# Kernel optimization log

Measured on AMD Instinct MI355X. Metric: run time of the kernel, lower is better.

Reference implementation:

```python
import jax, jax.numpy as jnp
import numpy as np

B, N, DH = 8, 2048, 512
EPS = 1e-5


def _layer_norm(x, g, b):
    m = x.mean(-1, keepdims=True)
    v = ((x - m) ** 2).mean(-1, keepdims=True)
    return (x - m) * jax.lax.rsqrt(v + EPS) * g + b


def setup_inputs() -> dict:
    key = jax.random.key(0)
    ks = jax.random.split(key, 20)
    s = 1.0 / np.sqrt(DH)
    sf = 1.0 / np.sqrt(2 * DH)
    return {
        "H": jax.random.normal(ks[0], (B, N, DH), jnp.float32),
        "adj": jax.random.uniform(ks[1], (B, N, N), jnp.float32),
        "hop_emb": jax.random.normal(ks[2], (N, DH), jnp.float32),
        "Wq": jax.random.normal(ks[3], (DH, DH), jnp.float32) * s,
        "bq": jnp.zeros((DH,), jnp.float32),
        "Wk": jax.random.normal(ks[4], (DH, DH), jnp.float32) * s,
        "bk": jnp.zeros((DH,), jnp.float32),
        "Wv": jax.random.normal(ks[5], (DH, DH), jnp.float32) * s,
        "bv": jnp.zeros((DH,), jnp.float32),
        "W1": jax.random.normal(ks[6], (DH, 2 * DH), jnp.float32) * s,
        "b1": jnp.zeros((2 * DH,), jnp.float32),
        "W2": jax.random.normal(ks[7], (2 * DH, DH), jnp.float32) * sf,
        "b2": jnp.zeros((DH,), jnp.float32),
        "g1": jnp.ones((DH,), jnp.float32),
        "be1": jnp.zeros((DH,), jnp.float32),
        "g2": jnp.ones((DH,), jnp.float32),
        "be2": jnp.zeros((DH,), jnp.float32),
    }


def reference(H, adj, hop_emb, Wq, bq, Wk, bk, Wv, bv, W1, b1, W2, b2, g1, be1, g2, be2):
    Q = H @ Wq + bq                                     # [B,N,DH]
    K = H @ Wk + bk
    V = H @ Wv + bv
    scores = jnp.einsum("bid,bjd->bij", Q, K) / np.sqrt(DH).astype(np.float32)
    # (adj[...,None] * hop_emb).mean(-1) == adj * hop_emb.mean(-1)[j]
    hop_effect = adj * hop_emb.mean(-1)[None, None, :]  # [B,N,N]
    attn = jax.nn.softmax(scores * hop_effect, axis=-1)
    attn_out = jnp.einsum("bij,bjd->bid", attn, V)
    x = _layer_norm(attn_out + H, g1, be1)
    ffn = jax.nn.relu(x @ W1 + b1) @ W2 + b2
    return _layer_norm(ffn + x, g2, be2)
```

## Files before the change

### kernel.cpp

```cpp
#include <hip/hip_runtime.h>

typedef unsigned short u16;
typedef __bf16 bf16x8 __attribute__((ext_vector_type(8)));
typedef float f32x4 __attribute__((ext_vector_type(4)));

#define SEQN 2048
#define DHID 512

static __device__ __forceinline__ float bf2f(u16 u) {
    union { unsigned int i; float f; } c; c.i = ((unsigned int)u) << 16; return c.f;
}
static __device__ __forceinline__ u16 f2bf(float f) {
    union { float f; unsigned int i; } c; c.f = f;
    unsigned int x = c.i;
    return (u16)((x + 0x7fffu + ((x >> 16) & 1u)) >> 16);
}

static __device__ __forceinline__ void gld_lds16(const u16* g, u16* l) {
    __builtin_amdgcn_global_load_lds(
        (__attribute__((address_space(1))) void*)(g),
        (__attribute__((address_space(3))) void*)(l), 16, 0, 0);
}

__global__ __launch_bounds__(256) void cvt_kernel(const float* __restrict__ src,
                                                  u16* __restrict__ dst, int n) {
    int i = (blockIdx.x * 256 + threadIdx.x) * 8;
    if (i >= n) return;
    float4 a = *(const float4*)(src + i);
    float4 b = *(const float4*)(src + i + 4);
    union { uint4 u; u16 s[8]; } o;
    o.s[0] = f2bf(a.x); o.s[1] = f2bf(a.y); o.s[2] = f2bf(a.z); o.s[3] = f2bf(a.w);
    o.s[4] = f2bf(b.x); o.s[5] = f2bf(b.y); o.s[6] = f2bf(b.z); o.s[7] = f2bf(b.w);
    *(uint4*)(dst + i) = o.u;
}

__global__ __launch_bounds__(256) void cvt_t_kernel(const float* __restrict__ src,
                                                    u16* __restrict__ dst, int K, int N) {
    int idx = blockIdx.x * 256 + threadIdx.x;
    if (idx >= K * N) return;
    int n = idx / K, k = idx - n * K;
    dst[idx] = f2bf(src[(size_t)k * N + n]);
}

__global__ void hmean_kernel(const float* __restrict__ hop, float* __restrict__ hm) {
    int j = blockIdx.x, t = threadIdx.x;
    const float* p = hop + (size_t)j * DHID + t * 8;
    float4 a = *(const float4*)p;
    float4 b = *(const float4*)(p + 4);
    float s = a.x + a.y + a.z + a.w + b.x + b.y + b.z + b.w;
#pragma unroll
    for (int m = 1; m < 64; m <<= 1) s += __shfl_xor(s, m);
    if (t == 0) hm[j] = s * (1.0f / (float)DHID);
}

enum { EPI_BIAS = 0, EPI_RELU = 1, EPI_PLAIN = 3, EPI_BIAS_T = 4, EPI_QKV = 5 };

template <int EPI>
__global__ __launch_bounds__(256) void gemm_bt(
    const u16* __restrict__ A, const u16* __restrict__ Bt, u16* __restrict__ C,
    const float* __restrict__ bias,
    int K, int lda, int ldb, int ldc,
    u16* __restrict__ Qo, u16* __restrict__ Ko, u16* __restrict__ Vto,
    const float* __restrict__ bq_, const float* __restrict__ bk_,
    const float* __restrict__ bv_)
{
    __shared__ u16 As[2][128 * 32];
    __shared__ u16 Bs[2][128 * 32];

    const int tid = threadIdx.x;
    const u16* Ab = A;
    const u16* Bb = Bt;

    const int bm0 = blockIdx.y * 128, bn0 = blockIdx.x * 128;
    const int wid = tid >> 6, lane = tid & 63, quad = lane >> 4, l16 = lane & 15;
    const int wm = (wid >> 1) * 64, wn = (wid & 1) * 64;
    const int srow = lane >> 2;
    const int skof = (lane & 3) * 8;

    f32x4 acc[4][4];
#pragma unroll
    for (int i = 0; i < 4; ++i)
#pragma unroll
        for (int j = 0; j < 4; ++j) acc[i][j] = (f32x4){0.f, 0.f, 0.f, 0.f};

#pragma unroll
    for (int it = 0; it < 2; ++it) {
        int c = wid * 2 + it;
        gld_lds16(Ab + (size_t)(bm0 + c * 16 + srow) * lda + skof, &As[0][c * 512]);
    }
#pragma unroll
    for (int it = 0; it < 2; ++it) {
        int c = wid * 2 + it;
        gld_lds16(Bb + (size_t)(bn0 + c * 16 + srow) * ldb + skof, &Bs[0][c * 512]);
    }

    int cur = 0;
    for (int k0 = 0; k0 < K; k0 += 32, cur ^= 1) {
        __syncthreads();

        if (k0 + 32 < K) {
#pragma unroll
            for (int it = 0; it < 2; ++it) {
                int c = wid * 2 + it;
                gld_lds16(Ab + (size_t)(bm0 + c * 16 + srow) * lda + k0 + 32 + skof,
                          &As[cur ^ 1][c * 512]);
            }
#pragma unroll
            for (int it = 0; it < 2; ++it) {
                int c = wid * 2 + it;
                gld_lds16(Bb + (size_t)(bn0 + c * 16 + srow) * ldb + k0 + 32 + skof,
                          &Bs[cur ^ 1][c * 512]);
            }
        }
        __builtin_amdgcn_sched_barrier(0);

        bf16x8 af[4], bfr[4];
#pragma unroll
        for (int i = 0; i < 4; ++i)
            af[i] = *(const bf16x8*)&As[cur][(wm + i * 16 + l16) * 32 + quad * 8];
#pragma unroll
        for (int j = 0; j < 4; ++j)
            bfr[j] = *(const bf16x8*)&Bs[cur][(wn + j * 16 + l16) * 32 + quad * 8];
#pragma unroll
        for (int i = 0; i < 4; ++i)
#pragma unroll
            for (int j = 0; j < 4; ++j)
                acc[i][j] = __builtin_amdgcn_mfma_f32_16x16x32_bf16(af[i], bfr[j], acc[i][j], 0, 0, 0);
    }

#pragma unroll
    for (int i = 0; i < 4; ++i) {
#pragma unroll
        for (int j = 0; j < 4; ++j) {
            const int gn = bn0 + wn + j * 16 + l16;
            const int gm0 = bm0 + wm + i * 16 + quad * 4;
            if constexpr (EPI == EPI_BIAS || EPI == EPI_RELU) {
                const float b = bias[gn];
#pragma unroll
                for (int r = 0; r < 4; ++r) {
                    float v = acc[i][j][r] + b;
                    if constexpr (EPI == EPI_RELU) v = fmaxf(v, 0.f);
                    C[(size_t)(gm0 + r) * ldc + gn] = f2bf(v);
                }
            } else if constexpr (EPI == EPI_BIAS_T) {
                const float b = bias[gn];
                const int bb = gm0 >> 11, n = gm0 & 2047;
                ushort4 o;
                o.x = f2bf(acc[i][j][0] + b);
                o.y = f2bf(acc[i][j][1] + b);
                o.z = f2bf(acc[i][j][2] + b);
                o.w = f2bf(acc[i][j][3] + b);
                *(ushort4*)&C[((size_t)bb * 512 + gn) * 2048 + n] = o;
            } else if constexpr (EPI == EPI_QKV) {
                const int sel = gn >> 9;
                const int n = gn & 511;
                if (sel == 0) {
                    const float b = bq_[n];
#pragma unroll
                    for (int r = 0; r < 4; ++r)
                        Qo[(size_t)(gm0 + r) * DHID + n] = f2bf(acc[i][j][r] + b);
                } else if (sel == 1) {
                    const float b = bk_[n];
#pragma unroll
                    for (int r = 0; r < 4; ++r)
                        Ko[(size_t)(gm0 + r) * DHID + n] = f2bf(acc[i][j][r] + b);
                } else {
                    const float b = bv_[n];
                    const int bb = gm0 >> 11, nn2 = gm0 & 2047;
                    ushort4 o;
                    o.x = f2bf(acc[i][j][0] + b);
                    o.y = f2bf(acc[i][j][1] + b);
                    o.z = f2bf(acc[i][j][2] + b);
                    o.w = f2bf(acc[i][j][3] + b);
                    *(ushort4*)&Vto[((size_t)bb * 512 + n) * 2048 + nn2] = o;
                }
            } else {
#pragma unroll
                for (int r = 0; r < 4; ++r)
                    C[(size_t)(gm0 + r) * ldc + gn] = f2bf(acc[i][j][r]);
            }
        }
    }
}

__global__ __launch_bounds__(256, 2) void attn_kernel(
    const u16* __restrict__ Q, const u16* __restrict__ K, const u16* __restrict__ Vt,
    const float* __restrict__ adj, const float* __restrict__ hm,
    u16* __restrict__ AO)
{
    extern __shared__ u16 lds[];
    u16* Ks = lds;
    u16* Vs = lds + 16384;
    u16* Pb = lds + 32768;

    const int tid = threadIdx.x, wid = tid >> 6, lane = tid & 63;
    const int quad = lane >> 4, l16 = lane & 15;
    const int b = blockIdx.x;
    const int q0 = blockIdx.y * 32 + (wid >> 1) * 16;
    const int ch = wid & 1;
    const int D0 = ch * 256;
    const int srow = lane >> 2, sko = (lane & 3) * 8;

    const u16* Qg = Q + (size_t)b * SEQN * DHID;
    const u16* Kg = K + (size_t)b * SEQN * DHID;
    const u16* Vg = Vt + (size_t)b * DHID * SEQN;
    const float* adjg = adj + (size_t)b * SEQN * SEQN;
    u16* AOg = AO + (size_t)b * SEQN * DHID;
    const float* arow = adjg + (size_t)(q0 + quad * 4) * SEQN;
    u16* Pg = Pb + (wid >> 1) * 640;

    const float scale = 0.044194173824159216f;

    bf16x8 qf[16];
#pragma unroll
    for (int ds = 0; ds < 16; ++ds)
        qf[ds] = *(const bf16x8*)(Qg + (size_t)(q0 + l16) * DHID + ds * 32 + quad * 8);

    f32x4 oacc[16];
#pragma unroll
    for (int dt = 0; dt < 16; ++dt) oacc[dt] = (f32x4){0.f, 0.f, 0.f, 0.f};
    float lsum[4] = {0.f, 0.f, 0.f, 0.f};

#pragma unroll
    for (int i = 0; i < 8; ++i) {
        int id = wid * 8 + i, ds = id >> 1, c = id & 1;
        gld_lds16(Kg + (size_t)(c * 16 + srow) * DHID + ds * 32 + sko,
                  &Ks[ds * 1024 + c * 512]);
    }

    for (int kt = 0; kt < 64; ++kt) {
        const int kv0 = kt * 32;

        __syncthreads();

#pragma unroll
        for (int i = 0; i < 8; ++i) {
            int id = wid * 8 + i;
            gld_lds16(Vg + (size_t)(id * 16 + srow) * SEQN + kv0 + sko,
                      &Vs[id * 512]);
        }

        float hv = hm[kv0 + ch * 16 + l16] * scale;
        float av[4];
#pragma unroll
        for (int r = 0; r < 4; ++r)
            av[r] = arow[(size_t)r * SEQN + kv0 + ch * 16 + l16];

        f32x4 sa = {0.f,0.f,0.f,0.f}, sb = {0.f,0.f,0.f,0.f};
#pragma unroll
        for (int ds = 0; ds < 16; ds += 2) {
            bf16x8 k0 = *(const bf16x8*)&Ks[ds * 1024 + ch * 512 + l16 * 32 + quad * 8];
            sa = __builtin_amdgcn_mfma_f32_16x16x32_bf16(qf[ds], k0, sa, 0, 0, 0);
            bf16x8 k1 = *(const bf16x8*)&Ks[(ds + 1) * 1024 + ch * 512 + l16 * 32 + quad * 8];
            sb = __builtin_amdgcn_mfma_f32_16x16x32_bf16(qf[ds + 1], k1, sb, 0, 0, 0);
        }
        f32x4 s = sa + sb;

        __syncthreads();

        if (kt < 63) {
#pragma unroll
            for (int i = 0; i < 8; ++i) {
                int id = wid * 8 + i, ds = id >> 1, c = id & 1;
                gld_lds16(Kg + (size_t)(kv0 + 32 + c * 16 + srow) * DHID + ds * 32 + sko,
                          &Ks[ds * 1024 + c * 512]);
            }
        }
        __builtin_amdgcn_sched_barrier(0);

#pragma unroll
        for (int r = 0; r < 4; ++r) {
            float p = __expf(s[r] * av[r] * hv);
            lsum[r] += p;
            Pg[(quad * 4 + r) * 40 + ch * 16 + l16] = f2bf(p);
        }

        asm volatile("s_waitcnt lgkmcnt(0)" ::: "memory");
        __builtin_amdgcn_s_barrier();
        __builtin_amdgcn_sched_barrier(0);

        bf16x8 pf = *(const bf16x8*)&Pg[l16 * 40 + quad * 8];

#pragma unroll
        for (int dt = 0; dt < 16; ++dt) {
            bf16x8 vf = *(const bf16x8*)&Vs[(D0 + dt * 16 + l16) * 32 + quad * 8];
            oacc[dt] = __builtin_amdgcn_mfma_f32_16x16x32_bf16(pf, vf, oacc[dt], 0, 0, 0);
        }
    }

#pragma unroll
    for (int r = 0; r < 4; ++r) {
#pragma unroll
        for (int m = 1; m < 16; m <<= 1) lsum[r] += __shfl_xor(lsum[r], m);
    }
    __syncthreads();
    float* SUMS = (float*)Pb;
    if (l16 == 0) {
#pragma unroll
        for (int r = 0; r < 4; ++r) SUMS[wid * 16 + quad * 4 + r] = lsum[r];
    }
    __syncthreads();
#pragma unroll
    for (int r = 0; r < 4; ++r)
        lsum[r] = 1.f / (lsum[r] + SUMS[(wid ^ 1) * 16 + quad * 4 + r]);

#pragma unroll
    for (int dt = 0; dt < 16; ++dt) {
#pragma unroll
        for (int r = 0; r < 4; ++r) {
            AOg[(size_t)(q0 + quad * 4 + r) * DHID + D0 + dt * 16 + l16] =
                f2bf(oacc[dt][r] * lsum[r]);
        }
    }
}

__global__ __launch_bounds__(256) void ln_hf32_kernel(
    const u16* __restrict__ a, const float* __restrict__ Hf,
    const float* __restrict__ g, const float* __restrict__ be,
    u16* __restrict__ out)
{
    size_t row = blockIdx.x;
    int t = threadIdx.x, wid = t >> 6, lane = t & 63;
    unsigned int va = *(const unsigned int*)(a + row * (size_t)DHID + t * 2);
    float2 h = *(const float2*)(Hf + row * (size_t)DHID + t * 2);
    float x0 = bf2f((u16)(va & 0xffff)) + h.x;
    float x1 = bf2f((u16)(va >> 16)) + h.y;
    float s = x0 + x1, sq = x0 * x0 + x1 * x1;
#pragma unroll
    for (int m = 1; m < 64; m <<= 1) { s += __shfl_xor(s, m); sq += __shfl_xor(sq, m); }
    __shared__ float rs[4], rq[4];
    if (lane == 0) { rs[wid] = s; rq[wid] = sq; }
    __syncthreads();
    s = rs[0] + rs[1] + rs[2] + rs[3];
    sq = rq[0] + rq[1] + rq[2] + rq[3];
    float mean = s * (1.f / (float)DHID);
    float var = sq * (1.f / (float)DHID) - mean * mean;
    float rstd = rsqrtf(var + 1e-5f);
    float2 vg = *(const float2*)(g + t * 2);
    float2 vbe = *(const float2*)(be + t * 2);
    float y0 = (x0 - mean) * rstd * vg.x + vbe.x;
    float y1 = (x1 - mean) * rstd * vg.y + vbe.y;
    unsigned int o = (unsigned int)f2bf(y0) | ((unsigned int)f2bf(y1) << 16);
    *(unsigned int*)(out + row * (size_t)DHID + t * 2) = o;
}

__global__ __launch_bounds__(256) void ln_kernel_f32out(
    const u16* __restrict__ a, const u16* __restrict__ bp,
    const float* __restrict__ g, const float* __restrict__ be,
    float* __restrict__ out)
{
    size_t row = blockIdx.x;
    int t = threadIdx.x, wid = t >> 6, lane = t & 63;
    unsigned int va = *(const unsigned int*)(a + row * (size_t)DHID + t * 2);
    unsigned int vb = *(const unsigned int*)(bp + row * (size_t)DHID + t * 2);
    float x0 = bf2f((u16)(va & 0xffff)) + bf2f((u16)(vb & 0xffff));
    float x1 = bf2f((u16)(va >> 16)) + bf2f((u16)(vb >> 16));
    float s = x0 + x1, sq = x0 * x0 + x1 * x1;
#pragma unroll
    for (int m = 1; m < 64; m <<= 1) { s += __shfl_xor(s, m); sq += __shfl_xor(sq, m); }
    __shared__ float rs[4], rq[4];
    if (lane == 0) { rs[wid] = s; rq[wid] = sq; }
    __syncthreads();
    s = rs[0] + rs[1] + rs[2] + rs[3];
    sq = rq[0] + rq[1] + rq[2] + rq[3];
    float mean = s * (1.f / (float)DHID);
    float var = sq * (1.f / (float)DHID) - mean * mean;
    float rstd = rsqrtf(var + 1e-5f);
    float2 vg = *(const float2*)(g + t * 2);
    float2 vbe = *(const float2*)(be + t * 2);
    float y0 = (x0 - mean) * rstd * vg.x + vbe.x;
    float y1 = (x1 - mean) * rstd * vg.y + vbe.y;
    *(float2*)(out + row * (size_t)DHID + t * 2) = make_float2(y0, y1);
}

extern "C" void kernel_launch(void* const* d_in, const int* in_sizes, int n_in,
                              void* d_out, int out_size, void* d_ws, size_t ws_size,
                              hipStream_t stream) {
    const float* H   = (const float*)d_in[0];
    const float* adj = (const float*)d_in[1];
    const float* hop = (const float*)d_in[2];
    const float* Wq  = (const float*)d_in[3];
    const float* bq  = (const float*)d_in[4];
    const float* Wk  = (const float*)d_in[5];
    const float* bk  = (const float*)d_in[6];
    const float* Wv  = (const float*)d_in[7];
    const float* bv  = (const float*)d_in[8];
    const float* W1  = (const float*)d_in[9];
    const float* b1  = (const float*)d_in[10];
    const float* W2  = (const float*)d_in[11];
    const float* b2  = (const float*)d_in[12];
    const float* g1  = (const float*)d_in[13];
    const float* be1 = (const float*)d_in[14];
    const float* g2  = (const float*)d_in[15];
    const float* be2 = (const float*)d_in[16];

    const size_t MiB = 1ull << 20;
    char* w = (char*)d_ws;
    float* hm   = (float*)w;
    u16* Hb    = (u16*)(w + 1 * MiB);
    u16* Wqkvt = (u16*)(w + 17 * MiB);
    u16* W1t   = (u16*)(w + 18 * MiB + 512 * 1024);
    u16* W2t   = (u16*)(w + 19 * MiB + 512 * 1024);
    u16* Q     = (u16*)(w + 21 * MiB);
    u16* Kb    = (u16*)(w + 37 * MiB);
    u16* Vt    = (u16*)(w + 53 * MiB);
    u16* AO    = (u16*)(w + 69 * MiB);
    u16* HID   = (u16*)(w + 85 * MiB);
    u16* X   = Kb;
    u16* F2  = Vt;

    const int BN = 8, N = SEQN, D = DHID;

    cvt_kernel<<<(BN * N * D) / (8 * 256), 256, 0, stream>>>(H, Hb, BN * N * D);
    cvt_t_kernel<<<(D * D + 255) / 256, 256, 0, stream>>>(Wq, Wqkvt, D, D);
    cvt_t_kernel<<<(D * D + 255) / 256, 256, 0, stream>>>(Wk, Wqkvt + D * D, D, D);
    cvt_t_kernel<<<(D * D + 255) / 256, 256, 0, stream>>>(Wv, Wqkvt + 2 * D * D, D, D);
    cvt_t_kernel<<<(D * 2 * D + 255) / 256, 256, 0, stream>>>(W1, W1t, D, 2 * D);
    cvt_t_kernel<<<(2 * D * D + 255) / 256, 256, 0, stream>>>(W2, W2t, 2 * D, D);

    hmean_kernel<<<N, 64, 0, stream>>>(hop, hm);

    gemm_bt<EPI_QKV><<<dim3(12, 128, 1), 256, 0, stream>>>(
        Hb, Wqkvt, nullptr, nullptr, D, D, D, 0, Q, Kb, Vt, bq, bk, bv);

    attn_kernel<<<dim3(8, 64), 256, 68096, stream>>>(Q, Kb, Vt, adj, hm, AO);

    ln_hf32_kernel<<<BN * N, 256, 0, stream>>>(AO, H, g1, be1, X);

    gemm_bt<EPI_RELU><<<dim3(8, 128, 1), 256, 0, stream>>>(
        X, W1t, HID, b1, D, D, D, 2 * D, nullptr, nullptr, nullptr, nullptr, nullptr, nullptr);

    gemm_bt<EPI_BIAS><<<dim3(4, 128, 1), 256, 0, stream>>>(
        HID, W2t, F2, b2, 2 * D, 2 * D, 2 * D, D, nullptr, nullptr, nullptr, nullptr, nullptr, nullptr);

    ln_kernel_f32out<<<BN * N, 256, 0, stream>>>(F2, X, g2, be2, (float*)d_out);
}
```

Baseline: 549.8 us.

## Fuse residual+LayerNorm into attention epilogue and merge prep kernels

```diff
diff --git a/kernel.cpp b/kernel.cpp
--- a/kernel.cpp
+++ b/kernel.cpp
@@ -22,35 +22,49 @@
         (__attribute__((address_space(3))) void*)(l), 16, 0, 0);
 }
 
-__global__ __launch_bounds__(256) void cvt_kernel(const float* __restrict__ src,
-                                                  u16* __restrict__ dst, int n) {
-    int i = (blockIdx.x * 256 + threadIdx.x) * 8;
-    if (i >= n) return;
-    float4 a = *(const float4*)(src + i);
-    float4 b = *(const float4*)(src + i + 4);
-    union { uint4 u; u16 s[8]; } o;
-    o.s[0] = f2bf(a.x); o.s[1] = f2bf(a.y); o.s[2] = f2bf(a.z); o.s[3] = f2bf(a.w);
-    o.s[4] = f2bf(b.x); o.s[5] = f2bf(b.y); o.s[6] = f2bf(b.z); o.s[7] = f2bf(b.w);
-    *(uint4*)(dst + i) = o.u;
-}
-
-__global__ __launch_bounds__(256) void cvt_t_kernel(const float* __restrict__ src,
-                                                    u16* __restrict__ dst, int K, int N) {
-    int idx = blockIdx.x * 256 + threadIdx.x;
-    if (idx >= K * N) return;
-    int n = idx / K, k = idx - n * K;
-    dst[idx] = f2bf(src[(size_t)k * N + n]);
-}
-
-__global__ void hmean_kernel(const float* __restrict__ hop, float* __restrict__ hm) {
-    int j = blockIdx.x, t = threadIdx.x;
-    const float* p = hop + (size_t)j * DHID + t * 8;
-    float4 a = *(const float4*)p;
-    float4 b = *(const float4*)(p + 4);
-    float s = a.x + a.y + a.z + a.w + b.x + b.y + b.z + b.w;
-#pragma unroll
-    for (int m = 1; m < 64; m <<= 1) s += __shfl_xor(s, m);
-    if (t == 0) hm[j] = s * (1.0f / (float)DHID);
+__global__ __launch_bounds__(256) void prep_kernel(
+    const float* __restrict__ H, const float* __restrict__ Wq,
+    const float* __restrict__ Wk, const float* __restrict__ Wv,
+    const float* __restrict__ W1, const float* __restrict__ W2,
+    const float* __restrict__ hop,
+    u16* __restrict__ Hb, u16* __restrict__ Wqkvt,
+    u16* __restrict__ W1t, u16* __restrict__ W2t, float* __restrict__ hm)
+{
+    const int bid = blockIdx.x, tid = threadIdx.x;
+    if (bid < 4096) {
+        int i = (bid * 256 + tid) * 8;
+        float4 a = *(const float4*)(H + i);
+        float4 c = *(const float4*)(H + i + 4);
+        union { uint4 u; u16 s[8]; } o;
+        o.s[0] = f2bf(a.x); o.s[1] = f2bf(a.y); o.s[2] = f2bf(a.z); o.s[3] = f2bf(a.w);
+        o.s[4] = f2bf(c.x); o.s[5] = f2bf(c.y); o.s[6] = f2bf(c.z); o.s[7] = f2bf(c.w);
+        *(uint4*)(Hb + i) = o.u;
+    } else if (bid < 7168) {
+        int idx = (bid - 4096) * 256 + tid;
+        int which = idx >> 18;
+        int rem = idx & 262143;
+        int n = rem >> 9, k = rem & 511;
+        const float* src = (which == 0) ? Wq : ((which == 1) ? Wk : Wv);
+        Wqkvt[idx] = f2bf(src[(size_t)k * 512 + n]);
+    } else if (bid < 9216) {
+        int idx = (bid - 7168) * 256 + tid;
+        int n = idx >> 9, k = idx & 511;
+        W1t[idx] = f2bf(W1[(size_t)k * 1024 + n]);
+    } else if (bid < 11264) {
+        int idx = (bid - 9216) * 256 + tid;
+        int n = idx >> 10, k = idx & 1023;
+        W2t[idx] = f2bf(W2[(size_t)k * 512 + n]);
+    } else {
+        int j = (bid - 11264) * 4 + (tid >> 6);
+        int lane = tid & 63;
+        const float* p = hop + (size_t)j * DHID + lane * 8;
+        float4 a = *(const float4*)p;
+        float4 c = *(const float4*)(p + 4);
+        float s = a.x + a.y + a.z + a.w + c.x + c.y + c.z + c.w;
+#pragma unroll
+        for (int m = 1; m < 64; m <<= 1) s += __shfl_xor(s, m);
+        if (lane == 0) hm[j] = s * (1.0f / (float)DHID);
+    }
 }
 
 enum { EPI_BIAS = 0, EPI_RELU = 1, EPI_PLAIN = 3, EPI_BIAS_T = 4, EPI_QKV = 5 };
@@ -142,15 +156,6 @@
                     if constexpr (EPI == EPI_RELU) v = fmaxf(v, 0.f);
                     C[(size_t)(gm0 + r) * ldc + gn] = f2bf(v);
                 }
-            } else if constexpr (EPI == EPI_BIAS_T) {
-                const float b = bias[gn];
-                const int bb = gm0 >> 11, n = gm0 & 2047;
-                ushort4 o;
-                o.x = f2bf(acc[i][j][0] + b);
-                o.y = f2bf(acc[i][j][1] + b);
-                o.z = f2bf(acc[i][j][2] + b);
-                o.w = f2bf(acc[i][j][3] + b);
-                *(ushort4*)&C[((size_t)bb * 512 + gn) * 2048 + n] = o;
             } else if constexpr (EPI == EPI_QKV) {
                 const int sel = gn >> 9;
                 const int n = gn & 511;
@@ -186,7 +191,8 @@
 __global__ __launch_bounds__(256, 2) void attn_kernel(
     const u16* __restrict__ Q, const u16* __restrict__ K, const u16* __restrict__ Vt,
     const float* __restrict__ adj, const float* __restrict__ hm,
-    u16* __restrict__ AO)
+    const float* __restrict__ Hf, const float* __restrict__ g1,
+    const float* __restrict__ be1, u16* __restrict__ X)
 {
     extern __shared__ u16 lds[];
     u16* Ks = lds;
@@ -205,7 +211,7 @@
     const u16* Kg = K + (size_t)b * SEQN * DHID;
     const u16* Vg = Vt + (size_t)b * DHID * SEQN;
     const float* adjg = adj + (size_t)b * SEQN * SEQN;
-    u16* AOg = AO + (size_t)b * SEQN * DHID;
+    u16* Xg = X + (size_t)b * SEQN * DHID;
     const float* arow = adjg + (size_t)(q0 + quad * 4) * SEQN;
     u16* Pg = Pb + (wid >> 1) * 640;
 
@@ -304,44 +310,54 @@
     for (int r = 0; r < 4; ++r)
         lsum[r] = 1.f / (lsum[r] + SUMS[(wid ^ 1) * 16 + quad * 4 + r]);
 
+    const float* Hfg = Hf + (size_t)b * SEQN * DHID;
+    float sr[4] = {0.f, 0.f, 0.f, 0.f}, sq[4] = {0.f, 0.f, 0.f, 0.f};
 #pragma unroll
     for (int dt = 0; dt < 16; ++dt) {
 #pragma unroll
         for (int r = 0; r < 4; ++r) {
-            AOg[(size_t)(q0 + quad * 4 + r) * DHID + D0 + dt * 16 + l16] =
-                f2bf(oacc[dt][r] * lsum[r]);
-        }
-    }
-}
-
-__global__ __launch_bounds__(256) void ln_hf32_kernel(
-    const u16* __restrict__ a, const float* __restrict__ Hf,
-    const float* __restrict__ g, const float* __restrict__ be,
-    u16* __restrict__ out)
-{
-    size_t row = blockIdx.x;
-    int t = threadIdx.x, wid = t >> 6, lane = t & 63;
-    unsigned int va = *(const unsigned int*)(a + row * (size_t)DHID + t * 2);
-    float2 h = *(const float2*)(Hf + row * (size_t)DHID + t * 2);
-    float x0 = bf2f((u16)(va & 0xffff)) + h.x;
-    float x1 = bf2f((u16)(va >> 16)) + h.y;
-    float s = x0 + x1, sq = x0 * x0 + x1 * x1;
-#pragma unroll
-    for (int m = 1; m < 64; m <<= 1) { s += __shfl_xor(s, m); sq += __shfl_xor(sq, m); }
-    __shared__ float rs[4], rq[4];
-    if (lane == 0) { rs[wid] = s; rq[wid] = sq; }
+            float h = Hfg[(size_t)(q0 + quad * 4 + r) * DHID + D0 + dt * 16 + l16];
+            float x = oacc[dt][r] * lsum[r] + h;
+            oacc[dt][r] = x;
+            sr[r] += x; sq[r] += x * x;
+        }
+    }
+#pragma unroll
+    for (int r = 0; r < 4; ++r) {
+#pragma unroll
+        for (int m = 1; m < 16; m <<= 1) {
+            sr[r] += __shfl_xor(sr[r], m);
+            sq[r] += __shfl_xor(sq[r], m);
+        }
+    }
     __syncthreads();
-    s = rs[0] + rs[1] + rs[2] + rs[3];
-    sq = rq[0] + rq[1] + rq[2] + rq[3];
-    float mean = s * (1.f / (float)DHID);
-    float var = sq * (1.f / (float)DHID) - mean * mean;
-    float rstd = rsqrtf(var + 1e-5f);
-    float2 vg = *(const float2*)(g + t * 2);
-    float2 vbe = *(const float2*)(be + t * 2);
-    float y0 = (x0 - mean) * rstd * vg.x + vbe.x;
-    float y1 = (x1 - mean) * rstd * vg.y + vbe.y;
-    unsigned int o = (unsigned int)f2bf(y0) | ((unsigned int)f2bf(y1) << 16);
-    *(unsigned int*)(out + row * (size_t)DHID + t * 2) = o;
+    if (l16 == 0) {
+#pragma unroll
+        for (int r = 0; r < 4; ++r) {
+            SUMS[(wid * 16 + quad * 4 + r) * 2]     = sr[r];
+            SUMS[(wid * 16 + quad * 4 + r) * 2 + 1] = sq[r];
+        }
+    }
+    __syncthreads();
+    float mean[4], rstd[4];
+#pragma unroll
+    for (int r = 0; r < 4; ++r) {
+        float S  = sr[r] + SUMS[((wid ^ 1) * 16 + quad * 4 + r) * 2];
+        float Q2 = sq[r] + SUMS[((wid ^ 1) * 16 + quad * 4 + r) * 2 + 1];
+        mean[r] = S * (1.f / (float)DHID);
+        float var = Q2 * (1.f / (float)DHID) - mean[r] * mean[r];
+        rstd[r] = rsqrtf(var + 1e-5f);
+    }
+#pragma unroll
+    for (int dt = 0; dt < 16; ++dt) {
+        float gv  = g1[D0 + dt * 16 + l16];
+        float bev = be1[D0 + dt * 16 + l16];
+#pragma unroll
+        for (int r = 0; r < 4; ++r) {
+            Xg[(size_t)(q0 + quad * 4 + r) * DHID + D0 + dt * 16 + l16] =
+                f2bf((oacc[dt][r] - mean[r]) * rstd[r] * gv + bev);
+        }
+    }
 }
 
 __global__ __launch_bounds__(256) void ln_kernel_f32out(
@@ -404,28 +420,20 @@
     u16* Q     = (u16*)(w + 21 * MiB);
     u16* Kb    = (u16*)(w + 37 * MiB);
     u16* Vt    = (u16*)(w + 53 * MiB);
-    u16* AO    = (u16*)(w + 69 * MiB);
+    u16* X     = (u16*)(w + 69 * MiB);
     u16* HID   = (u16*)(w + 85 * MiB);
-    u16* X   = Kb;
     u16* F2  = Vt;
 
     const int BN = 8, N = SEQN, D = DHID;
 
-    cvt_kernel<<<(BN * N * D) / (8 * 256), 256, 0, stream>>>(H, Hb, BN * N * D);
-    cvt_t_kernel<<<(D * D + 255) / 256, 256, 0, stream>>>(Wq, Wqkvt, D, D);
-    cvt_t_kernel<<<(D * D + 255) / 256, 256, 0, stream>>>(Wk, Wqkvt + D * D, D, D);
-    cvt_t_kernel<<<(D * D + 255) / 256, 256, 0, stream>>>(Wv, Wqkvt + 2 * D * D, D, D);
-    cvt_t_kernel<<<(D * 2 * D + 255) / 256, 256, 0, stream>>>(W1, W1t, D, 2 * D);
-    cvt_t_kernel<<<(2 * D * D + 255) / 256, 256, 0, stream>>>(W2, W2t, 2 * D, D);
-
-    hmean_kernel<<<N, 64, 0, stream>>>(hop, hm);
+    prep_kernel<<<11776, 256, 0, stream>>>(H, Wq, Wk, Wv, W1, W2, hop,
+                                           Hb, Wqkvt, W1t, W2t, hm);
 
     gemm_bt<EPI_QKV><<<dim3(12, 128, 1), 256, 0, stream>>>(
         Hb, Wqkvt, nullptr, nullptr, D, D, D, 0, Q, Kb, Vt, bq, bk, bv);
 
-    attn_kernel<<<dim3(8, 64), 256, 68096, stream>>>(Q, Kb, Vt, adj, hm, AO);
-
-    ln_hf32_kernel<<<BN * N, 256, 0, stream>>>(AO, H, g1, be1, X);
+    attn_kernel<<<dim3(8, 64), 256, 68096, stream>>>(Q, Kb, Vt, adj, hm,
+                                                     H, g1, be1, X);
 
     gemm_bt<EPI_RELU><<<dim3(8, 128, 1), 256, 0, stream>>>(
         X, W1t, HID, b1, D, D, D, 2 * D, nullptr, nullptr, nullptr, nullptr, nullptr, nullptr);
```

Measured after the change: 521.4 us. 5.2% less time.
